# Kernel optimization log

Hardware: AMD Instinct MI355X
Metric: run time of the kernel (lower is better)

Reference implementation:

```python
import jax, jax.numpy as jnp
import numpy as np

N_PRIORS = 262144
N_CLASSES = 81  # includes background at index 0


def _decode(loc, priors, variance):
    # Standard SSD decode: priors are [N,4] (cx, cy, w, h) in relative coords.
    centers = priors[:, :2] + loc[:, :2] * variance[0] * priors[:, 2:]
    sizes = priors[:, 2:] * jnp.exp(loc[:, 2:] * variance[1])
    mins = centers - sizes * 0.5          # (xmin, ymin)
    maxs = mins + sizes                   # (xmax, ymax)
    return jnp.concatenate([mins, maxs], axis=-1)  # [N,4]


def setup_inputs() -> dict:
    key = jax.random.key(0)
    k1, k2, k3 = jax.random.split(key, 3)
    inp = jax.random.normal(k1, (1, N_PRIORS, 4 + N_CLASSES), dtype=jnp.float32)
    cxy = jax.random.uniform(k2, (N_PRIORS, 2), dtype=jnp.float32)
    wh = jax.random.uniform(k3, (N_PRIORS, 2), dtype=jnp.float32) * 0.1 + 0.05
    priors = jnp.concatenate([cxy, wh], axis=-1)
    variance = jnp.array([0.1, 0.2], dtype=jnp.float32)
    score_threshold = jnp.array([0.3], dtype=jnp.float32)
    return {"input": inp, "priors": priors, "variance": variance,
            "score_threshold": score_threshold}


def reference(input, priors, variance, score_threshold):
    # input: [1, N, 4+C]
    loc = input[0, :, :4]                                   # [N,4]
    cls = jax.nn.softmax(input[0, :, 4:], axis=-1)          # [N,C]
    class_conf = jnp.max(cls, axis=1)                       # [N]
    class_pred = jnp.argmax(cls, axis=1)                    # [N] int
    boxes = _decode(loc, priors, variance)                  # [N,4]
    # torch version compacts via nonzero/index_select; jit-compatible
    # equivalent: keep fixed length N and mask out invalid rows.
    valid = (class_pred > 0) & (class_conf > score_threshold[0])  # [N] bool
    boxes = jnp.where(valid[:, None], boxes, 0.0)
    class_conf = jnp.where(valid, class_conf, 0.0)
    class_pred_out = jnp.where(valid, class_pred - 1, -1)
    detections = jnp.concatenate(
        [boxes, class_conf[:, None], class_pred_out[:, None].astype(jnp.float32)],
        axis=-1)                                            # [N,6]
    return boxes, class_conf, class_pred_out, detections[None]
```

## Files before the change

kernel.cpp:

```cpp
#include <hip/hip_runtime.h>

#define NCLS 81
#define ROW  85
#define TPB  64
#define CHUNK_F4 1360

__device__ __forceinline__ float exp_cr(float xf) {
    double x = (double)xf;
    x = (x < -150.0) ? -150.0 : x;
    double t = x * 1.4426950408889634074;
    double nd = rint(t);
    double r = fma(nd, -6.93147180369123816490e-01, x);
    r = fma(nd, -1.90821492927058770002e-10, r);
    double p = 1.0 / 6227020800.0;
    p = fma(p, r, 1.0 / 479001600.0);
    p = fma(p, r, 1.0 / 39916800.0);
    p = fma(p, r, 1.0 / 3628800.0);
    p = fma(p, r, 1.0 / 362880.0);
    p = fma(p, r, 1.0 / 40320.0);
    p = fma(p, r, 1.0 / 5040.0);
    p = fma(p, r, 1.0 / 720.0);
    p = fma(p, r, 1.0 / 120.0);
    p = fma(p, r, 1.0 / 24.0);
    p = fma(p, r, 1.0 / 6.0);
    p = fma(p, r, 0.5);
    p = fma(p, r, 1.0);
    p = fma(p, r, 1.0);
    long long ni = (long long)nd;
    double sc = __longlong_as_double((1023LL + ni) << 52);
    return (float)(p * sc);
}

__global__ __launch_bounds__(TPB) void ssd_decode_kernel(
    const float* __restrict__ inp,
    const float* __restrict__ priors,
    const float* __restrict__ var,
    const float* __restrict__ thr,
    float* __restrict__ out,
    int n)
{
    __shared__ __align__(16) float lds[TPB * ROW];
    const int tid = threadIdx.x;
    const long long base = (long long)blockIdx.x * TPB;
    if (base >= n) return;

    {
        const float4* g4 = reinterpret_cast<const float4*>(inp)
                         + (long long)blockIdx.x * CHUNK_F4;
        float4 v[21];
        #pragma unroll
        for (int k = 0; k < 21; ++k) v[k] = g4[k * TPB + tid];
        float vt = inp[(long long)blockIdx.x * (TPB * ROW) + 21 * 4 * TPB + tid];
        float4* l4 = reinterpret_cast<float4*>(lds);
        #pragma unroll
        for (int k = 0; k < 21; ++k) l4[k * TPB + tid] = v[k];
        lds[21 * 4 * TPB + tid] = vt;
    }
    __syncthreads();

    float* row = lds + tid * ROW;

    float lg[ROW];
    #pragma unroll
    for (int k = 0; k < ROW; ++k) lg[k] = row[k];

    float mx[8];
    #pragma unroll
    for (int j = 0; j < 8; ++j) mx[j] = lg[4 + j];
    #pragma unroll
    for (int k = 1; k < 10; ++k)
        #pragma unroll
        for (int j = 0; j < 8; ++j) mx[j] = fmaxf(mx[j], lg[4 + k * 8 + j]);
    float m = fmaxf(fmaxf(fmaxf(mx[0], mx[1]), fmaxf(mx[2], mx[3])),
                    fmaxf(fmaxf(mx[4], mx[5]), fmaxf(mx[6], mx[7])));
    m = fmaxf(m, lg[84]);

    int nc = 0;
    int amf = 127;
    float racc[8];
    #pragma unroll
    for (int j = 0; j < 8; ++j) racc[j] = 0.0f;
    #pragma unroll
    for (int k = 0; k < 10; ++k)
        #pragma unroll
        for (int j = 0; j < 8; ++j) {
            int c = k * 8 + j;
            float d = lg[4 + c] - m;
            nc  += (d >= -9.5367431640625e-07f) ? 1 : 0;
            int cand = (d == 0.0f) ? c : 127;
            amf = (cand < amf) ? cand : amf;
            racc[j] += __expf(d);
        }
    float s1 = ((racc[0] + racc[1]) + (racc[2] + racc[3]))
             + ((racc[4] + racc[5]) + (racc[6] + racc[7]));
    {
        float d80 = lg[84] - m;
        nc  += (d80 >= -9.5367431640625e-07f) ? 1 : 0;
        int cand = (d80 == 0.0f) ? 80 : 127;
        amf = (cand < amf) ? cand : amf;
        s1 += __expf(d80);
    }

    int am;
    float conf;
    if (__any(nc > 1)) {
        float racx[8];
        #pragma unroll
        for (int j = 0; j < 8; ++j) racx[j] = 0.0f;
        #pragma unroll
        for (int k = 0; k < 10; ++k)
            #pragma unroll
            for (int j = 0; j < 8; ++j) {
                float e = exp_cr(row[4 + k * 8 + j] - m);
                row[4 + k * 8 + j] = e;
                racx[j] += e;
            }
        float s = ((racx[0] + racx[1]) + (racx[2] + racx[3]))
                + ((racx[4] + racx[5]) + (racx[6] + racx[7]));
        float e80 = exp_cr(row[84] - m);
        row[84] = e80;
        s += e80;

        float pmax = 1.0f / s;
        float t = 1.0f;
        #pragma unroll
        for (int k = 0; k < 8; ++k) {
            float tn = __uint_as_float(__float_as_uint(t) - 1u);
            t = ((tn / s) == pmax) ? tn : t;
        }
        am = 81;
        #pragma unroll
        for (int c = 80; c >= 0; --c)
            am = (row[4 + c] >= t) ? c : am;
        conf = pmax;
    } else {
        am = amf;
        conf = 1.0f / s1;
    }

    float l0 = lg[0], l1 = lg[1], l2 = lg[2], l3 = lg[3];
    float4 pr = reinterpret_cast<const float4*>(priors)[base + tid];
    float v0 = var[0], v1 = var[1];
    float cx = pr.x + l0 * v0 * pr.z;
    float cy = pr.y + l1 * v0 * pr.w;
    float w  = pr.z * __expf(l2 * v1);
    float h  = pr.w * __expf(l3 * v1);
    float x0 = cx - w * 0.5f;
    float y0 = cy - h * 0.5f;
    float x1 = x0 + w;
    float y1 = y0 + h;

    bool valid = (am > 0) && (conf > thr[0]);

    float4 box;
    box.x = valid ? x0 : 0.0f;
    box.y = valid ? y0 : 0.0f;
    box.z = valid ? x1 : 0.0f;
    box.w = valid ? y1 : 0.0f;
    float cz = valid ? conf : 0.0f;
    float pz = valid ? (float)(am - 1) : -1.0f;

    const long long i = base + tid;
    reinterpret_cast<float4*>(out)[i] = box;
    out[(long long)4 * n + i] = cz;
    out[(long long)5 * n + i] = pz;
    float2* det2 = reinterpret_cast<float2*>(out + (long long)6 * n + i * 6);
    det2[0] = make_float2(box.x, box.y);
    det2[1] = make_float2(box.z, box.w);
    det2[2] = make_float2(cz, pz);
}

extern "C" void kernel_launch(void* const* d_in, const int* in_sizes, int n_in,
                              void* d_out, int out_size, void* d_ws, size_t ws_size,
                              hipStream_t stream)
{
    const float* inp    = (const float*)d_in[0];
    const float* priors = (const float*)d_in[1];
    const float* var    = (const float*)d_in[2];
    const float* thr    = (const float*)d_in[3];
    float* out = (float*)d_out;

    int n = in_sizes[1] / 4;
    int blocks = (n + TPB - 1) / TPB;
    ssd_decode_kernel<<<blocks, TPB, 0, stream>>>(inp, priors, var, thr, out, n);
}
```

Baseline: 142.9 us.

## Load softmax rows directly from global memory instead of staging through LDS

Removes the coalesced float4 staging of each block's rows into shared memory and the barrier. Each thread now reads its own 85-float row straight from global memory into registers, with 256 threads per block and a launch-bounds occupancy hint. The rare exact-tie path recomputes exp values rather than storing them back to LDS. Per-thread strided row reads (340-byte stride) are poorly coalesced and depend on the cache to merge accesses, so achieved memory bandwidth may fall.

```diff
diff --git a/kernel.cpp b/kernel.cpp
--- a/kernel.cpp
+++ b/kernel.cpp
@@ -2,8 +2,7 @@
 
 #define NCLS 81
 #define ROW  85
-#define TPB  64
-#define CHUNK_F4 1360
+#define TPB  256
 
 __device__ __forceinline__ float exp_cr(float xf) {
     double x = (double)xf;
@@ -31,7 +30,7 @@
     return (float)(p * sc);
 }
 
-__global__ __launch_bounds__(TPB) void ssd_decode_kernel(
+__global__ __launch_bounds__(TPB, 4) void ssd_decode_kernel(
     const float* __restrict__ inp,
     const float* __restrict__ priors,
     const float* __restrict__ var,
@@ -39,27 +38,10 @@
     float* __restrict__ out,
     int n)
 {
-    __shared__ __align__(16) float lds[TPB * ROW];
-    const int tid = threadIdx.x;
-    const long long base = (long long)blockIdx.x * TPB;
-    if (base >= n) return;
+    const int i = blockIdx.x * TPB + threadIdx.x;
+    if (i >= n) return;
 
-    {
-        const float4* g4 = reinterpret_cast<const float4*>(inp)
-                         + (long long)blockIdx.x * CHUNK_F4;
-        float4 v[21];
-        #pragma unroll
-        for (int k = 0; k < 21; ++k) v[k] = g4[k * TPB + tid];
-        float vt = inp[(long long)blockIdx.x * (TPB * ROW) + 21 * 4 * TPB + tid];
-        float4* l4 = reinterpret_cast<float4*>(lds);
-        #pragma unroll
-        for (int k = 0; k < 21; ++k) l4[k * TPB + tid] = v[k];
-        lds[21 * 4 * TPB + tid] = vt;
-    }
-    __syncthreads();
-
-    float* row = lds + tid * ROW;
-
+    const float* row = inp + (long long)i * ROW;
     float lg[ROW];
     #pragma unroll
     for (int k = 0; k < ROW; ++k) lg[k] = row[k];
@@ -110,16 +92,11 @@
         #pragma unroll
         for (int k = 0; k < 10; ++k)
             #pragma unroll
-            for (int j = 0; j < 8; ++j) {
-                float e = exp_cr(row[4 + k * 8 + j] - m);
-                row[4 + k * 8 + j] = e;
-                racx[j] += e;
-            }
+            for (int j = 0; j < 8; ++j)
+                racx[j] += exp_cr(lg[4 + k * 8 + j] - m);
         float s = ((racx[0] + racx[1]) + (racx[2] + racx[3]))
                 + ((racx[4] + racx[5]) + (racx[6] + racx[7]));
-        float e80 = exp_cr(row[84] - m);
-        row[84] = e80;
-        s += e80;
+        s += exp_cr(lg[84] - m);
 
         float pmax = 1.0f / s;
         float t = 1.0f;
@@ -131,7 +108,7 @@
         am = 81;
         #pragma unroll
         for (int c = 80; c >= 0; --c)
-            am = (row[4 + c] >= t) ? c : am;
+            am = (exp_cr(lg[4 + c] - m) >= t) ? c : am;
         conf = pmax;
     } else {
         am = amf;
@@ -139,7 +116,7 @@
     }
 
     float l0 = lg[0], l1 = lg[1], l2 = lg[2], l3 = lg[3];
-    float4 pr = reinterpret_cast<const float4*>(priors)[base + tid];
+    float4 pr = reinterpret_cast<const float4*>(priors)[i];
     float v0 = var[0], v1 = var[1];
     float cx = pr.x + l0 * v0 * pr.z;
     float cy = pr.y + l1 * v0 * pr.w;
@@ -160,11 +137,10 @@
     float cz = valid ? conf : 0.0f;
     float pz = valid ? (float)(am - 1) : -1.0f;
 
-    const long long i = base + tid;
     reinterpret_cast<float4*>(out)[i] = box;
     out[(long long)4 * n + i] = cz;
     out[(long long)5 * n + i] = pz;
-    float2* det2 = reinterpret_cast<float2*>(out + (long long)6 * n + i * 6);
+    float2* det2 = reinterpret_cast<float2*>(out + (long long)6 * n + (long long)i * 6);
     det2[0] = make_float2(box.x, box.y);
     det2[1] = make_float2(box.z, box.w);
     det2[2] = make_float2(cz, pz);
```

Measured after the change: 181.9 us. 27.3% more time.
